# Kernel optimization log

Hardware: AMD Instinct MI355X
Metric: run time of the kernel (lower is better)

The kernel has to match this reference:

```python
import jax, jax.numpy as jnp
import numpy as np

# Module hyper-parameters (eval mode: remove_rand_on_eval=True => no random additional points)
B, H, C, E = 2, 8, 2048, 1024
D = 64          # head_size
KP = 8          # k (points per query per head)
P = 2 * KP      # num_points = k * 2**rank, rank = 1


def setup_inputs() -> dict:
    key = jax.random.key(0)
    ks = jax.random.split(key, 10)
    x = jax.random.normal(ks[0], (B, C, E), jnp.float32)
    attention_mask = jnp.ones((B, C), jnp.int32)  # accepted but unused, as in the torch forward
    # hyper() outputs (abstract in the class): continuous means in [0, C-1), positive sigmas, values
    means = jax.random.uniform(ks[1], (B, H, C, KP, 1), jnp.float32) * (C - 1)
    sigmas = jax.random.uniform(ks[2], (B, H, C, KP), jnp.float32) * 2.0 + 0.5
    values = jax.random.normal(ks[3], (B, H, C, KP), jnp.float32)
    s_in = 1.0 / np.sqrt(E).astype(np.float32)
    s_u = 1.0 / np.sqrt(H * D).astype(np.float32)
    Wk = jax.random.normal(ks[4], (E, H * D), jnp.float32) * s_in
    Wq = jax.random.normal(ks[5], (E, H * D), jnp.float32) * s_in
    Wv = jax.random.normal(ks[6], (E, H * D), jnp.float32) * s_in
    Wu = jax.random.normal(ks[7], (H * D, E), jnp.float32) * s_u
    bu = jnp.zeros((E,), jnp.float32)
    return dict(x=x, attention_mask=attention_mask, means=means, sigmas=sigmas,
                values=values, Wk=Wk, Wq=Wq, Wv=Wv, Wu=Wu, bu=bu)


def reference(x, attention_mask, means, sigmas, values, Wk, Wq, Wv, Wu, bu):
    b, c, e = x.shape
    h, d, kp, p = H, D, KP, P

    # ---- ngenerate (eval: only the 2**rank = 2 integer corners per mean, clamped in-range) ----
    m = means[..., 0]                                  # (b,h,c,k)
    i0 = jnp.clip(jnp.floor(m).astype(jnp.int32), 0, c - 1)
    i1 = jnp.clip(i0 + 1, 0, c - 1)
    idx = jnp.stack([i0, i1], axis=-1).reshape(b, h, c, p)   # (b,h,c,P)
    idx_fl = idx.astype(jnp.float32)

    # ---- densities: unnormalized Gaussian of each integer point under each of the k means ----
    diff = idx_fl[..., :, None] - m[..., None, :]            # (b,h,c,P,k)
    dens = jnp.exp(-0.5 * (diff / sigmas[..., None, :]) ** 2)

    # ---- nduplicates: zero densities of repeated index tuples (keep first occurrence) ----
    eq = idx[..., :, None] == idx[..., None, :]              # (b,h,c,P,P)
    earlier = jnp.tril(jnp.ones((p, p), bool), k=-1)         # q < p
    dup = jnp.any(eq & earlier, axis=-1)                     # (b,h,c,P)
    dens = jnp.where(dup[..., None], 0.0, dens)

    # normalize over dim=2 (context), exactly as the torch code does
    dens = dens / (dens.sum(axis=2, keepdims=True) + 1e-8)

    # density-weighted continuous values -> per-point weights
    weights = (values[..., None, :] * dens).sum(axis=-1)     # (b,h,c,P)

    # ---- projections ----
    inv_sqrt_d = 1.0 / np.sqrt(d).astype(np.float32)
    Kt = (x @ Wk).reshape(b, c, h, d).transpose(0, 2, 1, 3) * inv_sqrt_d  # (b,h,c,d)
    Qt = (x @ Wq).reshape(b, c, h, d).transpose(0, 2, 1, 3) * inv_sqrt_d
    Vt = (x @ Wv).reshape(b, c, h, d).transpose(0, 2, 1, 3)

    # ---- gather K/V at the sparse indices ----
    flat = idx.reshape(b, h, c * p, 1)
    Kg = jnp.take_along_axis(Kt, flat, axis=2).reshape(b, h, c, p, d)
    Vg = jnp.take_along_axis(Vt, flat, axis=2).reshape(b, h, c, p, d)

    dots = jnp.einsum('bhcd,bhcpd->bhcp', Qt, Kg)
    new_weights = jax.nn.softmax(weights * dots, axis=-1)    # (b,h,c,P)

    head_reps = jnp.einsum('bhcpd,bhcp->bhcd', Vg, new_weights)
    united = head_reps.transpose(0, 2, 1, 3).reshape(b, c, h * d)
    new_out = united @ Wu + bu

    # ---- scatter-add sparse weights into dense attention matrix ----
    bi = jnp.arange(b)[:, None, None, None]
    hi = jnp.arange(h)[None, :, None, None]
    ci = jnp.arange(c)[None, None, :, None]
    attentions = jnp.zeros((b, h, c, c), jnp.float32).at[bi, hi, ci, idx].add(new_weights)

    return new_out, attentions
```

## Files before the change

### kernel.cpp

```cpp
#include <hip/hip_runtime.h>
#include <math.h>
#include <stdint.h>

#define B_ 2
#define H_ 8
#define C_ 2048
#define E_ 1024
#define D_ 64
#define KP_ 8
#define P_ 16
#define HD_ 512
#define ROWS_ 32768
#define M_ 4096

typedef __bf16 bf16x8 __attribute__((ext_vector_type(8)));
typedef float f32x4 __attribute__((ext_vector_type(4)));
typedef uint16_t u16x8 __attribute__((ext_vector_type(8)));

__device__ inline uint16_t f2bf(float f) {
    union { float f; uint32_t u; } v; v.f = f;
    uint32_t u = v.u + 0x7FFF + ((v.u >> 16) & 1);
    return (uint16_t)(u >> 16);
}
__device__ inline float bf2f(uint16_t h) {
    union { uint32_t u; float f; } v; v.u = ((uint32_t)h) << 16;
    return v.f;
}

__device__ inline void gload16(const uint16_t* g, uint16_t* l) {
    __builtin_amdgcn_global_load_lds(
        (const __attribute__((address_space(1))) void*)g,
        (__attribute__((address_space(3))) void*)l, 16, 0, 0);
}

__global__ __launch_bounds__(256) void prep_kernel(
    const float* __restrict__ x,
    const float* __restrict__ Wq, const float* __restrict__ Wk,
    const float* __restrict__ Wv, const float* __restrict__ Wu,
    const float* __restrict__ means, const float* __restrict__ sigmas,
    uint16_t* __restrict__ xb, uint16_t* __restrict__ Wall,
    uint16_t* __restrict__ Wut, float* __restrict__ S)
{
    const int bx = blockIdx.x;
    if (bx < 2048) {
        const int i = (bx * 256 + threadIdx.x) * 8;
        const float4 a = *(const float4*)(x + i);
        const float4 b = *(const float4*)(x + i + 4);
        u16x8 o;
        o[0] = f2bf(a.x); o[1] = f2bf(a.y); o[2] = f2bf(a.z); o[3] = f2bf(a.w);
        o[4] = f2bf(b.x); o[5] = f2bf(b.y); o[6] = f2bf(b.z); o[7] = f2bf(b.w);
        *(u16x8*)(xb + i) = o;
        return;
    }
    if (bx < 4096) {
        const int t = bx - 2048;
        const int z = t >> 9;
        const float* in; uint16_t* out; int R, Cc; float scale;
        if (z == 0)      { in = Wq; out = Wall;               R = E_;  Cc = HD_; scale = 0.125f; }
        else if (z == 1) { in = Wk; out = Wall + 512 * 1024;  R = E_;  Cc = HD_; scale = 0.125f; }
        else if (z == 2) { in = Wv; out = Wall + 1024 * 1024; R = E_;  Cc = HD_; scale = 1.0f; }
        else             { in = Wu; out = Wut;                R = HD_; Cc = E_;  scale = 1.0f; }
        const int tiles_x = Cc >> 5;
        const int ti = t & 511;
        const int tx = ti % tiles_x;
        const int ty = ti / tiles_x;
        const int r0 = ty * 32, c0 = tx * 32;
        __shared__ float tbuf[32][33];
        const int lx = threadIdx.x & 31, ly = threadIdx.x >> 5;
#pragma unroll
        for (int i = 0; i < 4; ++i)
            tbuf[ly * 4 + i][lx] = in[(size_t)(r0 + ly * 4 + i) * Cc + c0 + lx];
        __syncthreads();
#pragma unroll
        for (int i = 0; i < 4; ++i)
            out[(size_t)(c0 + ly * 4 + i) * R + r0 + lx] =
                f2bf(tbuf[lx][ly * 4 + i] * scale);
        return;
    }
    const int row = (bx - 4096) * 256 + threadIdx.x;
    const int lane = threadIdx.x & 63;
    const int bh = row >> 11;

    const float* mrow = means + (size_t)row * 8;
    const float* srow = sigmas + (size_t)row * 8;
    const float4 ma = *(const float4*)(mrow);
    const float4 mb = *(const float4*)(mrow + 4);
    const float4 sa = *(const float4*)(srow);
    const float4 sb = *(const float4*)(srow + 4);
    const float mm[8] = {ma.x, ma.y, ma.z, ma.w, mb.x, mb.y, mb.z, mb.w};
    const float sg[8] = {sa.x, sa.y, sa.z, sa.w, sb.x, sb.y, sb.z, sb.w};

    int idx[16];
#pragma unroll
    for (int j = 0; j < 8; ++j) {
        int i0 = (int)floorf(mm[j]);
        i0 = min(max(i0, 0), C_ - 1);
        idx[2 * j] = i0;
        idx[2 * j + 1] = min(i0 + 1, C_ - 1);
    }
    unsigned dupm = 0;
#pragma unroll
    for (int p = 1; p < 16; ++p) {
        bool d = false;
#pragma unroll
        for (int q = 0; q < 15; ++q)
            if (q < p) d = d || (idx[q] == idx[p]);
        if (d) dupm |= (1u << p);
    }
#pragma unroll
    for (int p = 0; p < 16; ++p) {
        const float fi = (float)idx[p];
        const bool dup = (dupm >> p) & 1u;
#pragma unroll
        for (int kk = 0; kk < 8; ++kk) {
            const float t = (fi - mm[kk]) / sg[kk];
            float val = dup ? 0.0f : expf(-0.5f * t * t);
#pragma unroll
            for (int off = 1; off < 64; off <<= 1)
                val += __shfl_xor(val, off);
            if (lane == 0)
                atomicAdd(&S[bh * 128 + p * 8 + kk], val);
        }
    }
}

__global__ __launch_bounds__(256) void gemm_qkv_kernel(
    const uint16_t* __restrict__ xb, const uint16_t* __restrict__ Wall,
    uint16_t* __restrict__ Qt, uint16_t* __restrict__ Kt,
    uint16_t* __restrict__ Vt)
{
    const int K = E_;
    const int m0 = blockIdx.y * 128;
    const int n0 = blockIdx.x * 64;
    const int z = n0 >> 9;
    uint16_t* __restrict__ Out = (z == 0) ? Qt : (z == 1) ? Kt : Vt;
    const int h = (n0 & 511) >> 6;

    __shared__ __align__(16) uint16_t smem[9216];
    uint16_t* As = smem;
    uint16_t* Bs = smem + 4096;

    const int tid = threadIdx.x;
    const int w = tid >> 6, lane = tid & 63;

    f32x4 acc[2][4] = {};

    const uint16_t* gP[3];
    uint16_t* lP[3];
#pragma unroll
    for (int j = 0; j < 3; ++j) {
        const int ci = w * 3 + j;
        const int rr = (ci & 7) * 16 + (lane >> 2);
        const int ko = (lane & 3) * 8;
        if (ci < 8) {
            gP[j] = xb + (size_t)(m0 + rr) * K + ko;
            lP[j] = &As[ci * 512];
        } else {
            const int cb = ci - 8;
            gP[j] = Wall + (size_t)(n0 + cb * 16 + (lane >> 2)) * K + ko;
            lP[j] = &Bs[cb * 512];
        }
    }

    const int fr = lane & 15;
    const int fk = (lane >> 4) * 8;

    for (int k0 = 0; k0 < K; k0 += 32) {
        __syncthreads();
        gload16(gP[0] + k0, lP[0]);
        gload16(gP[1] + k0, lP[1]);
        gload16(gP[2] + k0, lP[2]);
        __syncthreads();
        bf16x8 af[2], bf[4];
#pragma unroll
        for (int mt = 0; mt < 2; ++mt)
            af[mt] = *(const bf16x8*)&As[(w * 32 + mt * 16 + fr) * 32 + fk];
#pragma unroll
        for (int nt = 0; nt < 4; ++nt)
            bf[nt] = *(const bf16x8*)&Bs[(nt * 16 + fr) * 32 + fk];
#pragma unroll
        for (int mt = 0; mt < 2; ++mt)
#pragma unroll
            for (int nt = 0; nt < 4; ++nt)
                acc[mt][nt] = __builtin_amdgcn_mfma_f32_16x16x32_bf16(
                    af[mt], bf[nt], acc[mt][nt], 0, 0, 0);
    }

    __syncthreads();
#pragma unroll
    for (int mt = 0; mt < 2; ++mt)
#pragma unroll
        for (int nt = 0; nt < 4; ++nt) {
            const int col = nt * 16 + fr;
#pragma unroll
            for (int r = 0; r < 4; ++r) {
                const int rw = w * 32 + mt * 16 + (lane >> 4) * 4 + r;
                smem[rw * 72 + col] = f2bf(acc[mt][nt][r]);
            }
        }
    __syncthreads();
#pragma unroll
    for (int it = 0; it < 4; ++it) {
        const int j = it * 256 + tid;
        const int row = j >> 3, c8 = (j & 7) * 8;
        const int m = m0 + row;
        const int b = m >> 11, c = m & (C_ - 1);
        *(u16x8*)&Out[(((size_t)(b * H_ + h) * C_ + c) << 6) + c8] =
            *(const u16x8*)&smem[row * 72 + c8];
    }
}

__global__ __launch_bounds__(256) void gemm_out_kernel(
    const uint16_t* __restrict__ U, const uint16_t* __restrict__ Wut,
    const float* __restrict__ bu, float* __restrict__ out)
{
    const int K = HD_;
    const int m0 = blockIdx.y * 128;
    const int n0 = blockIdx.x * 64;

    __shared__ __align__(16) uint16_t As[128 * 32];
    __shared__ __align__(16) uint16_t Bs[64 * 32];

    const int tid = threadIdx.x;
    const int w = tid >> 6, lane = tid & 63;

    f32x4 acc[2][4] = {};

    const uint16_t* gP[3];
    uint16_t* lP[3];
#pragma unroll
    for (int j = 0; j < 3; ++j) {
        const int ci = w * 3 + j;
        const int ko = (lane & 3) * 8;
        if (ci < 8) {
            gP[j] = U + (size_t)(m0 + ci * 16 + (lane >> 2)) * K + ko;
            lP[j] = &As[ci * 512];
        } else {
            const int cb = ci - 8;
            gP[j] = Wut + (size_t)(n0 + cb * 16 + (lane >> 2)) * K + ko;
            lP[j] = &Bs[cb * 512];
        }
    }

    const int fr = lane & 15;
    const int fk = (lane >> 4) * 8;

    for (int k0 = 0; k0 < K; k0 += 32) {
        __syncthreads();
        gload16(gP[0] + k0, lP[0]);
        gload16(gP[1] + k0, lP[1]);
        gload16(gP[2] + k0, lP[2]);
        __syncthreads();
        bf16x8 af[2], bf[4];
#pragma unroll
        for (int mt = 0; mt < 2; ++mt)
            af[mt] = *(const bf16x8*)&As[(w * 32 + mt * 16 + fr) * 32 + fk];
#pragma unroll
        for (int nt = 0; nt < 4; ++nt)
            bf[nt] = *(const bf16x8*)&Bs[(nt * 16 + fr) * 32 + fk];
#pragma unroll
        for (int mt = 0; mt < 2; ++mt)
#pragma unroll
            for (int nt = 0; nt < 4; ++nt)
                acc[mt][nt] = __builtin_amdgcn_mfma_f32_16x16x32_bf16(
                    af[mt], bf[nt], acc[mt][nt], 0, 0, 0);
    }

#pragma unroll
    for (int mt = 0; mt < 2; ++mt) {
#pragma unroll
        for (int nt = 0; nt < 4; ++nt) {
            const int n = n0 + nt * 16 + fr;
            const float bias = bu[n];
#pragma unroll
            for (int r = 0; r < 4; ++r) {
                const int m = m0 + w * 32 + mt * 16 + (lane >> 4) * 4 + r;
                out[(size_t)m * E_ + n] = acc[mt][nt][r] + bias;
            }
        }
    }
}

__global__ __launch_bounds__(256) void attn_kernel(
    const float* __restrict__ means, const float* __restrict__ sigmas,
    const float* __restrict__ values, const float* __restrict__ S,
    const uint16_t* __restrict__ Qt, const uint16_t* __restrict__ Kt,
    const uint16_t* __restrict__ Vt, uint16_t* __restrict__ united,
    float* __restrict__ attn)
{
    __shared__ float rowbuf[4][2048];
    const int w = threadIdx.x >> 6;
    const int lane = threadIdx.x & 63;
    const int row = blockIdx.x * 4 + w;
    const int bh = row >> 11;
    const int c = row & (C_ - 1);
    const int b = bh >> 3;
    const int h = bh & 7;

    const float* mrow = means + (size_t)row * 8;
    const float4 ma = *(const float4*)(mrow);
    const float4 mb = *(const float4*)(mrow + 4);
    const float mm[8] = {ma.x, ma.y, ma.z, ma.w, mb.x, mb.y, mb.z, mb.w};

    int idx[16];
#pragma unroll
    for (int j = 0; j < 8; ++j) {
        int i0 = (int)floorf(mm[j]);
        i0 = min(max(i0, 0), C_ - 1);
        idx[2 * j] = i0;
        idx[2 * j + 1] = min(i0 + 1, C_ - 1);
    }

    const int lp = lane & 15;
    int myidx = 0;
#pragma unroll
    for (int q = 0; q < 16; ++q)
        if (q == lp) myidx = idx[q];
    float wp = 0.0f;
    if (lane < 16) {
        bool dup = false;
#pragma unroll
        for (int q = 0; q < 15; ++q)
            dup = dup || ((q < lane) && (idx[q] == myidx));
        if (!dup) {
            const float* srow = sigmas + (size_t)row * 8;
            const float* vrow = values + (size_t)row * 8;
            const float4 sa = *(const float4*)(srow);
            const float4 sb = *(const float4*)(srow + 4);
            const float4 va = *(const float4*)(vrow);
            const float4 vb = *(const float4*)(vrow + 4);
            const float sg[8] = {sa.x, sa.y, sa.z, sa.w, sb.x, sb.y, sb.z, sb.w};
            const float vl[8] = {va.x, va.y, va.z, va.w, vb.x, vb.y, vb.z, vb.w};
            const float* Sp = S + bh * 128 + lane * 8;
            const float4 Sa = *(const float4*)(Sp);
            const float4 Sb = *(const float4*)(Sp + 4);
            const float Sv[8] = {Sa.x, Sa.y, Sa.z, Sa.w, Sb.x, Sb.y, Sb.z, Sb.w};
            const float fi = (float)myidx;
#pragma unroll
            for (int kk = 0; kk < 8; ++kk) {
                const float t = (fi - mm[kk]) / sg[kk];
                const float e = expf(-0.5f * t * t);
                wp = fmaf(vl[kk], e / (Sv[kk] + 1e-8f), wp);
            }
        }
    }

    const int p = lane >> 2, g = lane & 3;
    int kidx = 0;
#pragma unroll
    for (int q = 0; q < 16; ++q)
        if (q == p) kidx = idx[q];

    const uint16_t* Qrow = Qt + ((size_t)row << 6);
    const uint16_t* Krow = Kt + ((((size_t)bh << 11) + kidx) << 6);
    const u16x8 qa = *(const u16x8*)(Qrow + g * 16);
    const u16x8 qb = *(const u16x8*)(Qrow + g * 16 + 8);
    const u16x8 ka = *(const u16x8*)(Krow + g * 16);
    const u16x8 kb = *(const u16x8*)(Krow + g * 16 + 8);
    float dot = 0.0f;
#pragma unroll
    for (int j = 0; j < 8; ++j) {
        dot = fmaf(bf2f(qa[j]), bf2f(ka[j]), dot);
        dot = fmaf(bf2f(qb[j]), bf2f(kb[j]), dot);
    }
    dot += __shfl_xor(dot, 1);
    dot += __shfl_xor(dot, 2);

    const float wvp = __shfl(wp, p);
    const float logit = wvp * dot;

    float mx = logit;
#pragma unroll
    for (int off = 4; off < 64; off <<= 1)
        mx = fmaxf(mx, __shfl_xor(mx, off));
    const float e = expf(logit - mx);
    float se = e;
#pragma unroll
    for (int off = 4; off < 64; off <<= 1)
        se += __shfl_xor(se, off);
    const float sm = e / se;

    float smv[16];
#pragma unroll
    for (int q = 0; q < 16; ++q)
        smv[q] = __shfl(sm, q * 4);
    const float myw = __shfl(sm, lp * 4);

    const uint16_t* Vbh = Vt + ((size_t)bh << 17);
    float acc = 0.0f;
#pragma unroll
    for (int q = 0; q < 16; ++q)
        acc = fmaf(bf2f(Vbh[((size_t)idx[q] << 6) + lane]), smv[q], acc);
    united[((size_t)(b * C_ + c)) * HD_ + h * 64 + lane] = f2bf(acc);

    const f32x4 z4 = {0.f, 0.f, 0.f, 0.f};
#pragma unroll
    for (int j = 0; j < 8; ++j)
        *(f32x4*)&rowbuf[w][(j * 64 + lane) * 4] = z4;
    __syncthreads();
    if (lane < 16) atomicAdd(&rowbuf[w][myidx], myw);
    __syncthreads();
    float* arow = attn + ((size_t)row << 11);
#pragma unroll
    for (int j = 0; j < 8; ++j) {
        const int o = (j * 64 + lane) * 4;
        __builtin_nontemporal_store(*(const f32x4*)&rowbuf[w][o], (f32x4*)&arow[o]);
    }
}

extern "C" void kernel_launch(void* const* d_in, const int* in_sizes, int n_in,
                              void* d_out, int out_size, void* d_ws,
                              size_t ws_size, hipStream_t stream) {
    const float* x      = (const float*)d_in[0];
    const float* means  = (const float*)d_in[2];
    const float* sigmas = (const float*)d_in[3];
    const float* values = (const float*)d_in[4];
    const float* Wk     = (const float*)d_in[5];
    const float* Wq     = (const float*)d_in[6];
    const float* Wv     = (const float*)d_in[7];
    const float* Wu     = (const float*)d_in[8];
    const float* bu     = (const float*)d_in[9];

    float* out  = (float*)d_out;
    float* attn = out + (size_t)M_ * E_;

    uint16_t* wsp = (uint16_t*)d_ws;
    uint16_t* xb     = wsp;
    uint16_t* Wall   = xb + 4194304;
    uint16_t* Wut    = Wall + 1572864;
    uint16_t* Qt     = Wut + 524288;
    uint16_t* Kt     = Qt + 2097152;
    uint16_t* Vt     = Kt + 2097152;
    uint16_t* united = Vt + 2097152;
    float*    S      = (float*)(united + 2097152);

    (void)hipMemsetAsync(S, 0, 2048 * sizeof(float), stream);

    prep_kernel<<<4224, 256, 0, stream>>>(
        x, Wq, Wk, Wv, Wu, means, sigmas, xb, Wall, Wut, S);
    gemm_qkv_kernel<<<dim3(24, 32), 256, 0, stream>>>(xb, Wall, Qt, Kt, Vt);
    attn_kernel<<<ROWS_ / 4, 256, 0, stream>>>(
        means, sigmas, values, S, Qt, Kt, Vt, united, attn);
    gemm_out_kernel<<<dim3(16, 32), 256, 0, stream>>>(united, Wut, bu, out);
}
```

Measured before the change: 414.8 us.

## Transpose-reduce density sums, deepen GEMM k-step, spread weight computation across lanes

The density-normalizer stage replaces 128 separate full-wave shuffle reductions and global atomics per wave with a butterfly transpose-reduction, so each lane ends up holding one (p,kk) sum. These sums are accumulated in shared memory and flushed to global with one atomic per slot per block. Both GEMMs now stage 64 K-columns per barrier pair, using two 32-wide halves of a larger LDS buffer, which halves the number of syncs. The attention kernel computes the sparse weights on all 64 lanes, each lane handling two of the eight mixture components, instead of 16 lanes doing all eight serially. The cost is more registers in the reduction (a 64-float array) and more LDS per GEMM block.

After: 387.3 us. 6.6% less time.

```diff
diff --git a/kernel.cpp b/kernel.cpp
--- a/kernel.cpp
+++ b/kernel.cpp
@@ -81,6 +81,10 @@
     const int lane = threadIdx.x & 63;
     const int bh = row >> 11;
 
+    __shared__ float Sacc[128];
+    if (threadIdx.x < 128) Sacc[threadIdx.x] = 0.0f;
+    __syncthreads();
+
     const float* mrow = means + (size_t)row * 8;
     const float* srow = sigmas + (size_t)row * 8;
     const float4 ma = *(const float4*)(mrow);
@@ -107,21 +111,38 @@
             if (q < p) d = d || (idx[q] == idx[p]);
         if (d) dupm |= (1u << p);
     }
-#pragma unroll
-    for (int p = 0; p < 16; ++p) {
-        const float fi = (float)idx[p];
-        const bool dup = (dupm >> p) & 1u;
-#pragma unroll
-        for (int kk = 0; kk < 8; ++kk) {
+
+    const int rev = ((lane & 1) << 5) | ((lane & 2) << 3) | ((lane & 4) << 1) |
+                    ((lane & 8) >> 1) | ((lane & 16) >> 3) | ((lane & 32) >> 5);
+
+#pragma unroll
+    for (int ph = 0; ph < 2; ++ph) {
+        float a[64];
+#pragma unroll
+        for (int j = 0; j < 64; ++j) {
+            const int p = ph * 8 + (j >> 3);
+            const int kk = j & 7;
+            const float fi = (float)idx[p];
             const float t = (fi - mm[kk]) / sg[kk];
-            float val = dup ? 0.0f : expf(-0.5f * t * t);
-#pragma unroll
-            for (int off = 1; off < 64; off <<= 1)
-                val += __shfl_xor(val, off);
-            if (lane == 0)
-                atomicAdd(&S[bh * 128 + p * 8 + kk], val);
-        }
-    }
+            const float e = expf(-0.5f * t * t);
+            a[j] = ((dupm >> p) & 1u) ? 0.0f : e;
+        }
+#pragma unroll
+        for (int b = 0; b < 6; ++b) {
+            const int n = 32 >> b;
+            const bool hi = (lane >> b) & 1;
+#pragma unroll
+            for (int j = 0; j < n; ++j) {
+                float send = hi ? a[j] : a[j + n];
+                float recv = __shfl_xor(send, 1 << b);
+                a[j] = (hi ? a[j + n] : a[j]) + recv;
+            }
+        }
+        atomicAdd(&Sacc[ph * 64 + rev], a[0]);
+    }
+    __syncthreads();
+    if (threadIdx.x < 128)
+        atomicAdd(&S[bh * 128 + threadIdx.x], Sacc[threadIdx.x]);
 }
 
 __global__ __launch_bounds__(256) void gemm_qkv_kernel(
@@ -136,9 +157,7 @@
     uint16_t* __restrict__ Out = (z == 0) ? Qt : (z == 1) ? Kt : Vt;
     const int h = (n0 & 511) >> 6;
 
-    __shared__ __align__(16) uint16_t smem[9216];
-    uint16_t* As = smem;
-    uint16_t* Bs = smem + 4096;
+    __shared__ __align__(16) uint16_t smem[12288];
 
     const int tid = threadIdx.x;
     const int w = tid >> 6, lane = tid & 63;
@@ -154,36 +173,42 @@
         const int ko = (lane & 3) * 8;
         if (ci < 8) {
             gP[j] = xb + (size_t)(m0 + rr) * K + ko;
-            lP[j] = &As[ci * 512];
+            lP[j] = &smem[ci * 512];
         } else {
             const int cb = ci - 8;
             gP[j] = Wall + (size_t)(n0 + cb * 16 + (lane >> 2)) * K + ko;
-            lP[j] = &Bs[cb * 512];
+            lP[j] = &smem[4096 + cb * 512];
         }
     }
 
     const int fr = lane & 15;
     const int fk = (lane >> 4) * 8;
 
-    for (int k0 = 0; k0 < K; k0 += 32) {
+    for (int k0 = 0; k0 < K; k0 += 64) {
         __syncthreads();
-        gload16(gP[0] + k0, lP[0]);
-        gload16(gP[1] + k0, lP[1]);
-        gload16(gP[2] + k0, lP[2]);
+#pragma unroll
+        for (int j = 0; j < 3; ++j) {
+            gload16(gP[j] + k0, lP[j]);
+            gload16(gP[j] + k0 + 32, lP[j] + 6144);
+        }
         __syncthreads();
-        bf16x8 af[2], bf[4];
-#pragma unroll
-        for (int mt = 0; mt < 2; ++mt)
-            af[mt] = *(const bf16x8*)&As[(w * 32 + mt * 16 + fr) * 32 + fk];
-#pragma unroll
-        for (int nt = 0; nt < 4; ++nt)
-            bf[nt] = *(const bf16x8*)&Bs[(nt * 16 + fr) * 32 + fk];
-#pragma unroll
-        for (int mt = 0; mt < 2; ++mt)
+#pragma unroll
+        for (int half = 0; half < 2; ++half) {
+            const int base = half * 6144;
+            bf16x8 af[2], bf[4];
+#pragma unroll
+            for (int mt = 0; mt < 2; ++mt)
+                af[mt] = *(const bf16x8*)&smem[base + (w * 32 + mt * 16 + fr) * 32 + fk];
 #pragma unroll
             for (int nt = 0; nt < 4; ++nt)
-                acc[mt][nt] = __builtin_amdgcn_mfma_f32_16x16x32_bf16(
-                    af[mt], bf[nt], acc[mt][nt], 0, 0, 0);
+                bf[nt] = *(const bf16x8*)&smem[base + 4096 + (nt * 16 + fr) * 32 + fk];
+#pragma unroll
+            for (int mt = 0; mt < 2; ++mt)
+#pragma unroll
+                for (int nt = 0; nt < 4; ++nt)
+                    acc[mt][nt] = __builtin_amdgcn_mfma_f32_16x16x32_bf16(
+                        af[mt], bf[nt], acc[mt][nt], 0, 0, 0);
+        }
     }
 
     __syncthreads();
@@ -218,8 +243,7 @@
     const int m0 = blockIdx.y * 128;
     const int n0 = blockIdx.x * 64;
 
-    __shared__ __align__(16) uint16_t As[128 * 32];
-    __shared__ __align__(16) uint16_t Bs[64 * 32];
+    __shared__ __align__(16) uint16_t smem[12288];
 
     const int tid = threadIdx.x;
     const int w = tid >> 6, lane = tid & 63;
@@ -234,36 +258,42 @@
         const int ko = (lane & 3) * 8;
         if (ci < 8) {
             gP[j] = U + (size_t)(m0 + ci * 16 + (lane >> 2)) * K + ko;
-            lP[j] = &As[ci * 512];
+            lP[j] = &smem[ci * 512];
         } else {
             const int cb = ci - 8;
             gP[j] = Wut + (size_t)(n0 + cb * 16 + (lane >> 2)) * K + ko;
-            lP[j] = &Bs[cb * 512];
+            lP[j] = &smem[4096 + cb * 512];
         }
     }
 
     const int fr = lane & 15;
     const int fk = (lane >> 4) * 8;
 
-    for (int k0 = 0; k0 < K; k0 += 32) {
+    for (int k0 = 0; k0 < K; k0 += 64) {
         __syncthreads();
-        gload16(gP[0] + k0, lP[0]);
-        gload16(gP[1] + k0, lP[1]);
-        gload16(gP[2] + k0, lP[2]);
+#pragma unroll
+        for (int j = 0; j < 3; ++j) {
+            gload16(gP[j] + k0, lP[j]);
+            gload16(gP[j] + k0 + 32, lP[j] + 6144);
+        }
         __syncthreads();
-        bf16x8 af[2], bf[4];
-#pragma unroll
-        for (int mt = 0; mt < 2; ++mt)
-            af[mt] = *(const bf16x8*)&As[(w * 32 + mt * 16 + fr) * 32 + fk];
-#pragma unroll
-        for (int nt = 0; nt < 4; ++nt)
-            bf[nt] = *(const bf16x8*)&Bs[(nt * 16 + fr) * 32 + fk];
-#pragma unroll
-        for (int mt = 0; mt < 2; ++mt)
+#pragma unroll
+        for (int half = 0; half < 2; ++half) {
+            const int base = half * 6144;
+            bf16x8 af[2], bf[4];
+#pragma unroll
+            for (int mt = 0; mt < 2; ++mt)
+                af[mt] = *(const bf16x8*)&smem[base + (w * 32 + mt * 16 + fr) * 32 + fk];
 #pragma unroll
             for (int nt = 0; nt < 4; ++nt)
-                acc[mt][nt] = __builtin_amdgcn_mfma_f32_16x16x32_bf16(
-                    af[mt], bf[nt], acc[mt][nt], 0, 0, 0);
+                bf[nt] = *(const bf16x8*)&smem[base + 4096 + (nt * 16 + fr) * 32 + fk];
+#pragma unroll
+            for (int mt = 0; mt < 2; ++mt)
+#pragma unroll
+                for (int nt = 0; nt < 4; ++nt)
+                    acc[mt][nt] = __builtin_amdgcn_mfma_f32_16x16x32_bf16(
+                        af[mt], bf[nt], acc[mt][nt], 0, 0, 0);
+        }
     }
 
 #pragma unroll
@@ -311,45 +341,36 @@
         idx[2 * j + 1] = min(i0 + 1, C_ - 1);
     }
 
-    const int lp = lane & 15;
-    int myidx = 0;
-#pragma unroll
-    for (int q = 0; q < 16; ++q)
-        if (q == lp) myidx = idx[q];
-    float wp = 0.0f;
-    if (lane < 16) {
-        bool dup = false;
-#pragma unroll
-        for (int q = 0; q < 15; ++q)
-            dup = dup || ((q < lane) && (idx[q] == myidx));
-        if (!dup) {
-            const float* srow = sigmas + (size_t)row * 8;
-            const float* vrow = values + (size_t)row * 8;
-            const float4 sa = *(const float4*)(srow);
-            const float4 sb = *(const float4*)(srow + 4);
-            const float4 va = *(const float4*)(vrow);
-            const float4 vb = *(const float4*)(vrow + 4);
-            const float sg[8] = {sa.x, sa.y, sa.z, sa.w, sb.x, sb.y, sb.z, sb.w};
-            const float vl[8] = {va.x, va.y, va.z, va.w, vb.x, vb.y, vb.z, vb.w};
-            const float* Sp = S + bh * 128 + lane * 8;
-            const float4 Sa = *(const float4*)(Sp);
-            const float4 Sb = *(const float4*)(Sp + 4);
-            const float Sv[8] = {Sa.x, Sa.y, Sa.z, Sa.w, Sb.x, Sb.y, Sb.z, Sb.w};
-            const float fi = (float)myidx;
-#pragma unroll
-            for (int kk = 0; kk < 8; ++kk) {
-                const float t = (fi - mm[kk]) / sg[kk];
-                const float e = expf(-0.5f * t * t);
-                wp = fmaf(vl[kk], e / (Sv[kk] + 1e-8f), wp);
-            }
-        }
-    }
-
     const int p = lane >> 2, g = lane & 3;
     int kidx = 0;
 #pragma unroll
     for (int q = 0; q < 16; ++q)
         if (q == p) kidx = idx[q];
+
+    bool dup = false;
+#pragma unroll
+    for (int q = 0; q < 15; ++q)
+        dup = dup || ((q < p) && (idx[q] == kidx));
+
+    float mA = 0.f, mB = 0.f;
+#pragma unroll
+    for (int q = 0; q < 4; ++q)
+        if (q == g) { mA = mm[q]; mB = mm[q + 4]; }
+    const float* srow = sigmas + (size_t)row * 8;
+    const float* vrow = values + (size_t)row * 8;
+    const float* Sp = S + bh * 128 + p * 8;
+    const float sgA = srow[g], sgB = srow[g + 4];
+    const float vlA = vrow[g], vlB = vrow[g + 4];
+    const float SvA = Sp[g],   SvB = Sp[g + 4];
+    const float fi = (float)kidx;
+    const float tA = (fi - mA) / sgA;
+    const float tB = (fi - mB) / sgB;
+    const float eA = expf(-0.5f * tA * tA);
+    const float eB = expf(-0.5f * tB * tB);
+    float wp = dup ? 0.0f
+                   : fmaf(vlA, eA / (SvA + 1e-8f), vlB * eB / (SvB + 1e-8f));
+    wp += __shfl_xor(wp, 1);
+    wp += __shfl_xor(wp, 2);
 
     const uint16_t* Qrow = Qt + ((size_t)row << 6);
     const uint16_t* Krow = Kt + ((((size_t)bh << 11) + kidx) << 6);
@@ -366,8 +387,7 @@
     dot += __shfl_xor(dot, 1);
     dot += __shfl_xor(dot, 2);
 
-    const float wvp = __shfl(wp, p);
-    const float logit = wvp * dot;
+    const float logit = wp * dot;
 
     float mx = logit;
 #pragma unroll
@@ -384,7 +404,6 @@
 #pragma unroll
     for (int q = 0; q < 16; ++q)
         smv[q] = __shfl(sm, q * 4);
-    const float myw = __shfl(sm, lp * 4);
 
     const uint16_t* Vbh = Vt + ((size_t)bh << 17);
     float acc = 0.0f;
@@ -398,7 +417,7 @@
     for (int j = 0; j < 8; ++j)
         *(f32x4*)&rowbuf[w][(j * 64 + lane) * 4] = z4;
     __syncthreads();
-    if (lane < 16) atomicAdd(&rowbuf[w][myidx], myw);
+    if (g == 0) atomicAdd(&rowbuf[w][kidx], sm);
     __syncthreads();
     float* arow = attn + ((size_t)row << 11);
 #pragma unroll
```
